# Kernel optimization log

Measured on AMD Instinct MI355X. Metric: run time of the kernel, lower is better.

Reference implementation:

```python
import jax, jax.numpy as jnp
import numpy as np

N_NODES = 100000


def setup_inputs() -> dict:
    key = jax.random.key(0)
    ks = jax.random.split(key, 8)
    nfeat, hdim, nclass, E = 512, 64, 256, 3200000
    x = jax.random.normal(ks[0], (N_NODES, nfeat), dtype=jnp.float32)
    edge_index = jax.random.randint(ks[1], (2, E), 0, N_NODES, dtype=jnp.int64)
    Win = jax.random.normal(ks[2], (nfeat, hdim), dtype=jnp.float32) * (1.0 / np.sqrt(nfeat))
    b_in = jnp.zeros((hdim,), dtype=jnp.float32)
    Wl = jax.random.normal(ks[3], (4, hdim, hdim), dtype=jnp.float32) * (1.0 / np.sqrt(hdim))
    bl = jnp.zeros((4, hdim), dtype=jnp.float32)
    Wr = jax.random.normal(ks[4], (4, hdim, hdim), dtype=jnp.float32) * (1.0 / np.sqrt(hdim))
    Wout = jax.random.normal(ks[5], (hdim, nclass), dtype=jnp.float32) * (1.0 / np.sqrt(hdim))
    b_out = jnp.zeros((nclass,), dtype=jnp.float32)
    return {"x": x, "edge_index": edge_index, "Win": Win, "b_in": b_in,
            "Wl": Wl, "bl": bl, "Wr": Wr, "Wout": Wout, "b_out": b_out}


def reference(x, edge_index, Win, b_in, Wl, bl, Wr, Wout, b_out):
    src, dst = edge_index[0], edge_index[1]
    # in-degree counts for scatter-mean (clamped to >=1 as in PyG)
    cnt = jax.ops.segment_sum(jnp.ones((src.shape[0],), dtype=x.dtype), dst,
                              num_segments=N_NODES)
    inv_cnt = (1.0 / jnp.maximum(cnt, 1.0))[:, None]  # [N,1]

    h = x @ Win + b_in  # [N, 64]
    for i in range(4):
        msg = h[src]  # gather neighbor features [E, 64]
        agg = jax.ops.segment_sum(msg, dst, num_segments=N_NODES) * inv_cnt
        conv = agg @ Wl[i] + bl[i] + h @ Wr[i]  # SAGEConv: lin_l(agg) + lin_r(h)
        h = h + jax.nn.relu(conv)  # residual
    return h @ Wout + b_out
```

## Files before the change

kernel.cpp:

```cpp
#include <hip/hip_runtime.h>
#include <hip/hip_bf16.h>

#define NN 100000
#define EE 3200000
#define HD 64
#define NF 512
#define NC 256

#define BSH 8
#define NB 391
#define EB 8192
#define NEB 391

typedef __attribute__((ext_vector_type(8))) short bf16x8;
typedef __attribute__((ext_vector_type(4))) float f32x4;
typedef __attribute__((ext_vector_type(4))) unsigned short u16x4;

__device__ __forceinline__ unsigned short f2bf(float f) {
    unsigned u = __float_as_uint(f);
    return (unsigned short)((u + 0x7FFFu + ((u >> 16) & 1u)) >> 16);
}
__device__ __forceinline__ unsigned pack2(float a, float b) {
    return (unsigned)f2bf(a) | ((unsigned)f2bf(b) << 16);
}
__device__ __forceinline__ float bf2f(unsigned short v) {
    return __uint_as_float(((unsigned)v) << 16);
}


__global__ __launch_bounds__(256) void part_count(const int* __restrict__ dst, int* __restrict__ hist) {
    __shared__ int hs[NB];
    int t = threadIdx.x, blk = blockIdx.x;
    for (int b = t; b < NB; b += 256) hs[b] = 0;
    __syncthreads();
    int base = blk * EB;
#pragma unroll
    for (int i = 0; i < EB / 256; ++i) {
        int e = base + t + 256 * i;
        if (e < EE) atomicAdd(&hs[dst[e] >> BSH], 1);
    }
    __syncthreads();
    for (int b = t; b < NB; b += 256) hist[blk * NB + b] = hs[b];
}


__global__ __launch_bounds__(512) void bucket_ptr(const int* __restrict__ hist, int* __restrict__ bucketptr) {
    __shared__ int s[512];
    int t = threadIdx.x;
    int v = 0;
    if (t < NB) {
        for (int blk = 0; blk < NEB; ++blk) v += hist[blk * NB + t];
    }
    s[t] = v; __syncthreads();
    for (int d = 1; d < 512; d <<= 1) {
        int a = (t >= d) ? s[t - d] : 0;
        __syncthreads();
        s[t] += a;
        __syncthreads();
    }
    if (t < NB) bucketptr[t] = s[t] - v;
    if (t == 0) bucketptr[NB] = EE;
}


__global__ __launch_bounds__(512) void part_scan(const int* __restrict__ hist, const int* __restrict__ bucketptr,
                                                 int* __restrict__ bboff) {
    __shared__ int s[512];
    int b = blockIdx.x, t = threadIdx.x;
    int v = (t < NEB) ? hist[t * NB + b] : 0;
    s[t] = v; __syncthreads();
    for (int d = 1; d < 512; d <<= 1) {
        int a = (t >= d) ? s[t - d] : 0;
        __syncthreads();
        s[t] += a;
        __syncthreads();
    }
    if (t < NEB) bboff[t * NB + b] = bucketptr[b] + s[t] - v;
}


__global__ __launch_bounds__(256) void part_scatter(const int* __restrict__ src, const int* __restrict__ dst,
                                                    const int* __restrict__ bboff, unsigned int* __restrict__ ebuf) {
    __shared__ int off[NB];
    __shared__ int rank[NB];
    int t = threadIdx.x, blk = blockIdx.x;
    for (int b = t; b < NB; b += 256) { off[b] = bboff[blk * NB + b]; rank[b] = 0; }
    __syncthreads();
    int base = blk * EB;
#pragma unroll
    for (int i = 0; i < EB / 256; ++i) {
        int e = base + t + 256 * i;
        if (e < EE) {
            int d = dst[e];
            int s = src[e];
            int b = d >> BSH;
            int r = atomicAdd(&rank[b], 1);
            ebuf[off[b] + r] = (unsigned)s | ((unsigned)(d & 255) << 17);
        }
    }
}


__global__ __launch_bounds__(256) void bucket_fill2(const unsigned int* __restrict__ ebuf,
                                                    const int* __restrict__ bucketptr,
                                                    int* __restrict__ rowptr, float* __restrict__ inv,
                                                    int* __restrict__ csr) {
    __shared__ int hcnt[256];
    __shared__ int scn[256];
    __shared__ int cur[256];
    int t = threadIdx.x, b = blockIdx.x;
    int n0 = b << BSH;
    hcnt[t] = 0;
    __syncthreads();
    int estart = bucketptr[b];
    int eend = bucketptr[b + 1];
    for (int e = estart + t; e < eend; e += 256) {
        atomicAdd(&hcnt[ebuf[e] >> 17], 1);
    }
    __syncthreads();
    int v = hcnt[t];
    scn[t] = v;
    __syncthreads();
    for (int d = 1; d < 256; d <<= 1) {
        int a = (t >= d) ? scn[t - d] : 0;
        __syncthreads();
        scn[t] += a;
        __syncthreads();
    }
    int off = estart + scn[t] - v;
    cur[t] = off;
    if (n0 + t < NN) {
        rowptr[n0 + t] = off;
        inv[n0 + t] = 1.0f / (float)(v > 1 ? v : 1);
    }
    if (b == NB - 1 && t == 0) rowptr[NN] = EE;
    __syncthreads();
    for (int e = estart + t; e < eend; e += 256) {
        unsigned u = ebuf[e];
        int dL = (int)(u >> 17);
        int p = atomicAdd(&cur[dL], 1);
        csr[p] = (int)(u & 0x1FFFFu);
    }
}


__global__ __launch_bounds__(256) void pack_w(const float* __restrict__ Win, unsigned short* __restrict__ wpk) {
    int id = blockIdx.x * 256 + threadIdx.x;
    int l = id & 63;
    int c = (id >> 6) & 3;
    int t = id >> 8;
    int kbase = t * 32 + (l >> 4) * 8;
    int col = c * 16 + (l & 15);
    float f[8];
#pragma unroll
    for (int j = 0; j < 8; ++j) f[j] = Win[(size_t)(kbase + j) * HD + col];
    uint4 p;
    p.x = pack2(f[0], f[1]); p.y = pack2(f[2], f[3]);
    p.z = pack2(f[4], f[5]); p.w = pack2(f[6], f[7]);
    *(uint4*)(wpk + (size_t)id * 8) = p;
}


__global__ __launch_bounds__(256) void gemm_in(const float* __restrict__ x, const unsigned short* __restrict__ wpk,
                                               const float* __restrict__ b_in, float* __restrict__ h,
                                               unsigned short* __restrict__ hb) {
    __shared__ unsigned short xs[128 * 64];
    int tid = threadIdx.x;
    int lane = tid & 63;
    int w = tid >> 6;
    int rowBase = blockIdx.x * 128;
    int lr = lane & 15;
    int lg = lane >> 4;

    f32x4 acc[2][4];
#pragma unroll
    for (int c = 0; c < 4; ++c) {
        float bb = b_in[c * 16 + lr];
#pragma unroll
        for (int m = 0; m < 2; ++m) acc[m][c] = (f32x4){bb, bb, bb, bb};
    }

    for (int kt = 0; kt < NF; kt += 64) {
        __syncthreads();
#pragma unroll
        for (int i = 0; i < 4; ++i) {
            int idx = tid + 256 * i;
            int r = idx >> 3;
            int u = idx & 7;
            int grow = rowBase + r;
            if (grow >= NN) grow = NN - 1;
            const float* srcp = x + (size_t)grow * NF + kt + u * 8;
            float4 a = *(const float4*)(srcp);
            float4 b = *(const float4*)(srcp + 4);
            uint4 p;
            p.x = pack2(a.x, a.y); p.y = pack2(a.z, a.w);
            p.z = pack2(b.x, b.y); p.w = pack2(b.z, b.w);
            int u2 = u ^ (r & 7);
            *(uint4*)(xs + (size_t)r * 64 + u2 * 8) = p;
        }
        __syncthreads();
#pragma unroll
        for (int ks = 0; ks < 2; ++ks) {
            int tstep = (kt >> 5) + ks;
            bf16x8 av[2], bv[4];
#pragma unroll
            for (int m = 0; m < 2; ++m) {
                int r = w * 32 + m * 16 + lr;
                int u2 = (ks * 4 + lg) ^ (r & 7);
                av[m] = *(const bf16x8*)(xs + (size_t)r * 64 + u2 * 8);
            }
#pragma unroll
            for (int c = 0; c < 4; ++c) {
                bv[c] = *(const bf16x8*)(wpk + (((size_t)tstep * 4 + c) * 64 + lane) * 8);
            }
#pragma unroll
            for (int m = 0; m < 2; ++m)
#pragma unroll
                for (int c = 0; c < 4; ++c)
                    acc[m][c] = __builtin_amdgcn_mfma_f32_16x16x32_bf16(av[m], bv[c], acc[m][c], 0, 0, 0);
        }
    }

#pragma unroll
    for (int m = 0; m < 2; ++m) {
        int rbase = rowBase + w * 32 + m * 16 + lg * 4;
#pragma unroll
        for (int j = 0; j < 4; ++j) {
            int row = rbase + j;
            if (row < NN) {
#pragma unroll
                for (int c = 0; c < 4; ++c) {
                    float v = acc[m][c][j];
                    h[(size_t)row * HD + c * 16 + lr] = v;
                    hb[(size_t)row * HD + c * 16 + lr] = f2bf(v);
                }
            }
        }
    }
}


__global__ __launch_bounds__(256) void aggregate(const unsigned short* __restrict__ hb, const int* __restrict__ rowptr,
                                                 const int* __restrict__ csr, const float* __restrict__ inv,
                                                 float4* __restrict__ agg4) {
    int tid = threadIdx.x;
    int lane = tid & 63;
    int q = lane >> 4;
    int f = lane & 15;
    int node = blockIdx.x * 4 + (tid >> 6);
    int n = __builtin_amdgcn_readfirstlane(node);
    int start = rowptr[n];
    int end = rowptr[n + 1];

    float4 acc0 = make_float4(0.f, 0.f, 0.f, 0.f);
    float4 acc1 = make_float4(0.f, 0.f, 0.f, 0.f);
    int e = start;
    int end8 = start + ((end - start) & ~7);
    for (; e < end8; e += 8) {
        int s0 = csr[e + q];
        int s1 = csr[e + 4 + q];
        u16x4 v0 = *(const u16x4*)(hb + (size_t)s0 * HD + f * 4);
        u16x4 v1 = *(const u16x4*)(hb + (size_t)s1 * HD + f * 4);
        acc0.x += bf2f(v0.x); acc0.y += bf2f(v0.y); acc0.z += bf2f(v0.z); acc0.w += bf2f(v0.w);
        acc1.x += bf2f(v1.x); acc1.y += bf2f(v1.y); acc1.z += bf2f(v1.z); acc1.w += bf2f(v1.w);
    }
    if (e + q < end) {
        int s = csr[e + q];
        u16x4 v = *(const u16x4*)(hb + (size_t)s * HD + f * 4);
        acc0.x += bf2f(v.x); acc0.y += bf2f(v.y); acc0.z += bf2f(v.z); acc0.w += bf2f(v.w);
    }
    e += 4;
    if (e + q < end) {
        int s = csr[e + q];
        u16x4 v = *(const u16x4*)(hb + (size_t)s * HD + f * 4);
        acc1.x += bf2f(v.x); acc1.y += bf2f(v.y); acc1.z += bf2f(v.z); acc1.w += bf2f(v.w);
    }

    float4 a;
    a.x = acc0.x + acc1.x;
    a.y = acc0.y + acc1.y;
    a.z = acc0.z + acc1.z;
    a.w = acc0.w + acc1.w;
    a.x += __shfl_xor(a.x, 16); a.x += __shfl_xor(a.x, 32);
    a.y += __shfl_xor(a.y, 16); a.y += __shfl_xor(a.y, 32);
    a.z += __shfl_xor(a.z, 16); a.z += __shfl_xor(a.z, 32);
    a.w += __shfl_xor(a.w, 16); a.w += __shfl_xor(a.w, 32);

    if (q == 0) {
        float s = inv[n];
        float4 r;
        r.x = a.x * s; r.y = a.y * s; r.z = a.z * s; r.w = a.w * s;
        agg4[(size_t)n * 16 + f] = r;
    }
}


__global__ __launch_bounds__(256) void layer_conv(const float* __restrict__ agg, float* __restrict__ h,
                                                  unsigned short* __restrict__ hb,
                                                  const float* __restrict__ Wl, const float* __restrict__ Wr,
                                                  const float* __restrict__ bl) {
    __shared__ float as_[64 * 64];
    __shared__ float hs[64 * 64];
    int tid = threadIdx.x;
    int cg = tid & 15;
    int rg = tid >> 4;
    int rowBase = blockIdx.x * 64;
    float4 bb = *(const float4*)(bl + cg * 4);
    float acc[4][4];
#pragma unroll
    for (int r = 0; r < 4; ++r) {
        acc[r][0] = bb.x; acc[r][1] = bb.y; acc[r][2] = bb.z; acc[r][3] = bb.w;
    }

#pragma unroll
    for (int i = 0; i < 4; ++i) {
        int idx = tid + 256 * i;
        int r = idx >> 4;
        int c4 = idx & 15;
        int grow = rowBase + r;
        if (grow >= NN) grow = NN - 1;
        int c4s = c4 ^ ((r >> 2) & 3);
        *(float4*)(as_ + r * 64 + c4s * 4) = *(const float4*)(agg + (size_t)grow * HD + c4 * 4);
        *(float4*)(hs + r * 64 + c4s * 4) = *(const float4*)(h + (size_t)grow * HD + c4 * 4);
    }
    __syncthreads();

#pragma unroll 2
    for (int k = 0; k < 64; k += 4) {
        int kq = k >> 2;
        float4 l0 = *(const float4*)(Wl + (size_t)(k + 0) * HD + cg * 4);
        float4 l1 = *(const float4*)(Wl + (size_t)(k + 1) * HD + cg * 4);
        float4 l2 = *(const float4*)(Wl + (size_t)(k + 2) * HD + cg * 4);
        float4 l3 = *(const float4*)(Wl + (size_t)(k + 3) * HD + cg * 4);
        float4 r0 = *(const float4*)(Wr + (size_t)(k + 0) * HD + cg * 4);
        float4 r1 = *(const float4*)(Wr + (size_t)(k + 1) * HD + cg * 4);
        float4 r2 = *(const float4*)(Wr + (size_t)(k + 2) * HD + cg * 4);
        float4 r3 = *(const float4*)(Wr + (size_t)(k + 3) * HD + cg * 4);
#pragma unroll
        for (int r = 0; r < 4; ++r) {
            int row = rg * 4 + r;
            int c4s = kq ^ ((row >> 2) & 3);
            float4 av = *(const float4*)(as_ + row * 64 + c4s * 4);
            float4 hv = *(const float4*)(hs + row * 64 + c4s * 4);
            acc[r][0] = fmaf(av.x, l0.x, acc[r][0]);
            acc[r][1] = fmaf(av.x, l0.y, acc[r][1]);
            acc[r][2] = fmaf(av.x, l0.z, acc[r][2]);
            acc[r][3] = fmaf(av.x, l0.w, acc[r][3]);
            acc[r][0] = fmaf(av.y, l1.x, acc[r][0]);
            acc[r][1] = fmaf(av.y, l1.y, acc[r][1]);
            acc[r][2] = fmaf(av.y, l1.z, acc[r][2]);
            acc[r][3] = fmaf(av.y, l1.w, acc[r][3]);
            acc[r][0] = fmaf(av.z, l2.x, acc[r][0]);
            acc[r][1] = fmaf(av.z, l2.y, acc[r][1]);
            acc[r][2] = fmaf(av.z, l2.z, acc[r][2]);
            acc[r][3] = fmaf(av.z, l2.w, acc[r][3]);
            acc[r][0] = fmaf(av.w, l3.x, acc[r][0]);
            acc[r][1] = fmaf(av.w, l3.y, acc[r][1]);
            acc[r][2] = fmaf(av.w, l3.z, acc[r][2]);
            acc[r][3] = fmaf(av.w, l3.w, acc[r][3]);
            acc[r][0] = fmaf(hv.x, r0.x, acc[r][0]);
            acc[r][1] = fmaf(hv.x, r0.y, acc[r][1]);
            acc[r][2] = fmaf(hv.x, r0.z, acc[r][2]);
            acc[r][3] = fmaf(hv.x, r0.w, acc[r][3]);
            acc[r][0] = fmaf(hv.y, r1.x, acc[r][0]);
            acc[r][1] = fmaf(hv.y, r1.y, acc[r][1]);
            acc[r][2] = fmaf(hv.y, r1.z, acc[r][2]);
            acc[r][3] = fmaf(hv.y, r1.w, acc[r][3]);
            acc[r][0] = fmaf(hv.z, r2.x, acc[r][0]);
            acc[r][1] = fmaf(hv.z, r2.y, acc[r][1]);
            acc[r][2] = fmaf(hv.z, r2.z, acc[r][2]);
            acc[r][3] = fmaf(hv.z, r2.w, acc[r][3]);
            acc[r][0] = fmaf(hv.w, r3.x, acc[r][0]);
            acc[r][1] = fmaf(hv.w, r3.y, acc[r][1]);
            acc[r][2] = fmaf(hv.w, r3.z, acc[r][2]);
            acc[r][3] = fmaf(hv.w, r3.w, acc[r][3]);
        }
    }

#pragma unroll
    for (int r = 0; r < 4; ++r) {
        int row = rowBase + rg * 4 + r;
        if (row < NN) {
            int lrow = rg * 4 + r;
            int c4s = cg ^ ((lrow >> 2) & 3);
            float4 ho = *(const float4*)(hs + lrow * 64 + c4s * 4);
            float4 o;
            float c0 = acc[r][0], c1 = acc[r][1], c2 = acc[r][2], c3 = acc[r][3];
            o.x = ho.x + (c0 > 0.f ? c0 : 0.f);
            o.y = ho.y + (c1 > 0.f ? c1 : 0.f);
            o.z = ho.z + (c2 > 0.f ? c2 : 0.f);
            o.w = ho.w + (c3 > 0.f ? c3 : 0.f);
            *(float4*)(h + (size_t)row * HD + cg * 4) = o;
            u16x4 ob;
            ob.x = f2bf(o.x); ob.y = f2bf(o.y); ob.z = f2bf(o.z); ob.w = f2bf(o.w);
            *(u16x4*)(hb + (size_t)row * HD + cg * 4) = ob;
        }
    }
}


__global__ __launch_bounds__(256) void gemm_out_k(const float* __restrict__ h, const float* __restrict__ Wout,
                                                  const float* __restrict__ b_out, float* __restrict__ out) {
    __shared__ float hs[32 * 64];
    int tid = threadIdx.x;
    int cg = tid & 63;
    int rg = tid >> 6;
    int rowBase = blockIdx.x * 32;
#pragma unroll
    for (int i = 0; i < 2; ++i) {
        int idx = tid + 256 * i;
        int r = idx >> 4;
        int c4 = idx & 15;
        int grow = rowBase + r;
        if (grow >= NN) grow = NN - 1;
        *(float4*)(hs + r * 64 + c4 * 4) = *(const float4*)(h + (size_t)grow * HD + c4 * 4);
    }
    __syncthreads();

    float4 bb = *(const float4*)(b_out + cg * 4);
    float acc[8][4];
#pragma unroll
    for (int r = 0; r < 8; ++r) {
        acc[r][0] = bb.x; acc[r][1] = bb.y; acc[r][2] = bb.z; acc[r][3] = bb.w;
    }

#pragma unroll 2
    for (int k = 0; k < 64; k += 4) {
        float4 w0 = *(const float4*)(Wout + (size_t)(k + 0) * NC + cg * 4);
        float4 w1 = *(const float4*)(Wout + (size_t)(k + 1) * NC + cg * 4);
        float4 w2 = *(const float4*)(Wout + (size_t)(k + 2) * NC + cg * 4);
        float4 w3 = *(const float4*)(Wout + (size_t)(k + 3) * NC + cg * 4);
#pragma unroll
        for (int r = 0; r < 8; ++r) {
            float4 hv = *(const float4*)(hs + (rg * 8 + r) * 64 + k);
            acc[r][0] = fmaf(hv.x, w0.x, acc[r][0]);
            acc[r][1] = fmaf(hv.x, w0.y, acc[r][1]);
            acc[r][2] = fmaf(hv.x, w0.z, acc[r][2]);
            acc[r][3] = fmaf(hv.x, w0.w, acc[r][3]);
            acc[r][0] = fmaf(hv.y, w1.x, acc[r][0]);
            acc[r][1] = fmaf(hv.y, w1.y, acc[r][1]);
            acc[r][2] = fmaf(hv.y, w1.z, acc[r][2]);
            acc[r][3] = fmaf(hv.y, w1.w, acc[r][3]);
            acc[r][0] = fmaf(hv.z, w2.x, acc[r][0]);
            acc[r][1] = fmaf(hv.z, w2.y, acc[r][1]);
            acc[r][2] = fmaf(hv.z, w2.z, acc[r][2]);
            acc[r][3] = fmaf(hv.z, w2.w, acc[r][3]);
            acc[r][0] = fmaf(hv.w, w3.x, acc[r][0]);
            acc[r][1] = fmaf(hv.w, w3.y, acc[r][1]);
            acc[r][2] = fmaf(hv.w, w3.z, acc[r][2]);
            acc[r][3] = fmaf(hv.w, w3.w, acc[r][3]);
        }
    }
#pragma unroll
    for (int r = 0; r < 8; ++r) {
        int row = rowBase + rg * 8 + r;
        if (row < NN) {
            float4 o;
            o.x = acc[r][0]; o.y = acc[r][1]; o.z = acc[r][2]; o.w = acc[r][3];
            *(float4*)(out + (size_t)row * NC + cg * 4) = o;
        }
    }
}

extern "C" void kernel_launch(void* const* d_in, const int* in_sizes, int n_in,
                              void* d_out, int out_size, void* d_ws, size_t ws_size,
                              hipStream_t stream) {
    const float* x    = (const float*)d_in[0];
    const int*   ei   = (const int*)d_in[1];
    const float* Win  = (const float*)d_in[2];
    const float* b_in = (const float*)d_in[3];
    const float* Wl   = (const float*)d_in[4];
    const float* bl   = (const float*)d_in[5];
    const float* Wr   = (const float*)d_in[6];
    const float* Wout = (const float*)d_in[7];
    const float* b_out= (const float*)d_in[8];
    float* out = (float*)d_out;

    const int* src = ei;
    const int* dst = ei + EE;

    char* ws = (char*)d_ws;
    float* h        = (float*)ws;
    float* agg      = h + (size_t)NN * HD;
    int*   rowptr   = (int*)(agg + (size_t)NN * HD);
    int*   csr      = rowptr + 100004;
    float* inv      = (float*)(csr + EE);
    int*   bucketptr= (int*)(inv + NN);
    unsigned short* wpk = (unsigned short*)(bucketptr + 400);
    unsigned short* hbf = wpk + 32768;

    unsigned int* ebuf = (unsigned int*)agg;
    int* hist  = (int*)agg + EE;
    int* bboff = hist + NEB * NB;

    pack_w<<<16, 256, 0, stream>>>(Win, wpk);

    part_count<<<NEB, 256, 0, stream>>>(dst, hist);
    bucket_ptr<<<1, 512, 0, stream>>>(hist, bucketptr);
    part_scan<<<NB, 512, 0, stream>>>(hist, bucketptr, bboff);
    part_scatter<<<NEB, 256, 0, stream>>>(src, dst, bboff, ebuf);
    bucket_fill2<<<NB, 256, 0, stream>>>(ebuf, bucketptr, rowptr, inv, csr);

    gemm_in<<<(NN + 127) / 128, 256, 0, stream>>>(x, wpk, b_in, h, hbf);

    for (int i = 0; i < 4; ++i) {
        aggregate<<<NN / 4, 256, 0, stream>>>(hbf, rowptr, csr, inv, (float4*)agg);
        layer_conv<<<(NN + 63) / 64, 256, 0, stream>>>(agg, h, hbf, Wl + (size_t)i * HD * HD,
                                                       Wr + (size_t)i * HD * HD, bl + (size_t)i * HD);
    }

    gemm_out_k<<<(NN + 31) / 32, 256, 0, stream>>>(h, Wout, b_out, out);
}
```

Before: 1.004 ms.

## Fuse aggregation with SAGE conv via bf16 MFMA and use MFMA output GEMM

New measurement: 901.3 us. 10.2% less time.

```diff
diff --git a/kernel.cpp b/kernel.cpp
--- a/kernel.cpp
+++ b/kernel.cpp
@@ -42,7 +42,6 @@
     __syncthreads();
     for (int b = t; b < NB; b += 256) hist[blk * NB + b] = hs[b];
 }
-
 
 __global__ __launch_bounds__(512) void bucket_ptr(const int* __restrict__ hist, int* __restrict__ bucketptr) {
     __shared__ int s[512];
@@ -61,7 +60,6 @@
     if (t < NB) bucketptr[t] = s[t] - v;
     if (t == 0) bucketptr[NB] = EE;
 }
-
 
 __global__ __launch_bounds__(512) void part_scan(const int* __restrict__ hist, const int* __restrict__ bucketptr,
                                                  int* __restrict__ bboff) {
@@ -78,7 +76,6 @@
     if (t < NEB) bboff[t * NB + b] = bucketptr[b] + s[t] - v;
 }
 
-
 __global__ __launch_bounds__(256) void part_scatter(const int* __restrict__ src, const int* __restrict__ dst,
                                                     const int* __restrict__ bboff, unsigned int* __restrict__ ebuf) {
     __shared__ int off[NB];
@@ -99,7 +96,6 @@
         }
     }
 }
-
 
 __global__ __launch_bounds__(256) void bucket_fill2(const unsigned int* __restrict__ ebuf,
                                                     const int* __restrict__ bucketptr,
@@ -158,6 +154,44 @@
     p.x = pack2(f[0], f[1]); p.y = pack2(f[2], f[3]);
     p.z = pack2(f[4], f[5]); p.w = pack2(f[6], f[7]);
     *(uint4*)(wpk + (size_t)id * 8) = p;
+}
+
+__global__ __launch_bounds__(256) void pack_wl(const float* __restrict__ Wl, const float* __restrict__ Wr,
+                                               unsigned short* __restrict__ wlpk) {
+    int id = blockIdx.x * 256 + threadIdx.x;
+    int l = id & 63;
+    int c = (id >> 6) & 3;
+    int t = (id >> 8) & 3;
+    int i = id >> 10;
+    int kbase = t * 32 + (l >> 4) * 8;
+    int col = c * 16 + (l & 15);
+    float f[8];
+#pragma unroll
+    for (int j = 0; j < 8; ++j) {
+        int k = kbase + j;
+        f[j] = (k < 64) ? Wl[(size_t)i * 4096 + (size_t)k * HD + col]
+                        : Wr[(size_t)i * 4096 + (size_t)(k - 64) * HD + col];
+    }
+    uint4 p;
+    p.x = pack2(f[0], f[1]); p.y = pack2(f[2], f[3]);
+    p.z = pack2(f[4], f[5]); p.w = pack2(f[6], f[7]);
+    *(uint4*)(wlpk + (size_t)id * 8) = p;
+}
+
+__global__ __launch_bounds__(256) void pack_wout(const float* __restrict__ Wout, unsigned short* __restrict__ wopk) {
+    int id = blockIdx.x * 256 + threadIdx.x;
+    int l = id & 63;
+    int c = (id >> 6) & 15;
+    int t = id >> 10;
+    int kbase = t * 32 + (l >> 4) * 8;
+    int col = c * 16 + (l & 15);
+    float f[8];
+#pragma unroll
+    for (int j = 0; j < 8; ++j) f[j] = Wout[(size_t)(kbase + j) * NC + col];
+    uint4 p;
+    p.x = pack2(f[0], f[1]); p.y = pack2(f[2], f[3]);
+    p.z = pack2(f[4], f[5]); p.w = pack2(f[6], f[7]);
+    *(uint4*)(wopk + (size_t)id * 8) = p;
 }
 
 
@@ -240,17 +274,25 @@
 }
 
 
-__global__ __launch_bounds__(256) void aggregate(const unsigned short* __restrict__ hb, const int* __restrict__ rowptr,
-                                                 const int* __restrict__ csr, const float* __restrict__ inv,
-                                                 float4* __restrict__ agg4) {
+__global__ __launch_bounds__(1024) void layer_fused(const float* __restrict__ hin,
+                                                    const unsigned short* __restrict__ hbin,
+                                                    const int* __restrict__ rowptr, const int* __restrict__ csr,
+                                                    const float* __restrict__ inv,
+                                                    const unsigned short* __restrict__ wlpk,
+                                                    const float* __restrict__ bl,
+                                                    float* __restrict__ hout, unsigned short* __restrict__ hbout) {
+    __shared__ unsigned short a_bf[16 * 64];
+    __shared__ unsigned short h_bf[16 * 64];
+    __shared__ float h_f[16 * 64];
     int tid = threadIdx.x;
+    int w = tid >> 6;
     int lane = tid & 63;
+    int node = __builtin_amdgcn_readfirstlane(blockIdx.x * 16 + w);
+
     int q = lane >> 4;
     int f = lane & 15;
-    int node = blockIdx.x * 4 + (tid >> 6);
-    int n = __builtin_amdgcn_readfirstlane(node);
-    int start = rowptr[n];
-    int end = rowptr[n + 1];
+    int start = rowptr[node];
+    int end = rowptr[node + 1];
 
     float4 acc0 = make_float4(0.f, 0.f, 0.f, 0.f);
     float4 acc1 = make_float4(0.f, 0.f, 0.f, 0.f);
@@ -259,23 +301,22 @@
     for (; e < end8; e += 8) {
         int s0 = csr[e + q];
         int s1 = csr[e + 4 + q];
-        u16x4 v0 = *(const u16x4*)(hb + (size_t)s0 * HD + f * 4);
-        u16x4 v1 = *(const u16x4*)(hb + (size_t)s1 * HD + f * 4);
+        u16x4 v0 = *(const u16x4*)(hbin + (size_t)s0 * HD + f * 4);
+        u16x4 v1 = *(const u16x4*)(hbin + (size_t)s1 * HD + f * 4);
         acc0.x += bf2f(v0.x); acc0.y += bf2f(v0.y); acc0.z += bf2f(v0.z); acc0.w += bf2f(v0.w);
         acc1.x += bf2f(v1.x); acc1.y += bf2f(v1.y); acc1.z += bf2f(v1.z); acc1.w += bf2f(v1.w);
     }
     if (e + q < end) {
         int s = csr[e + q];
-        u16x4 v = *(const u16x4*)(hb + (size_t)s * HD + f * 4);
+        u16x4 v = *(const u16x4*)(hbin + (size_t)s * HD + f * 4);
         acc0.x += bf2f(v.x); acc0.y += bf2f(v.y); acc0.z += bf2f(v.z); acc0.w += bf2f(v.w);
     }
     e += 4;
     if (e + q < end) {
         int s = csr[e + q];
-        u16x4 v = *(const u16x4*)(hb + (size_t)s * HD + f * 4);
+        u16x4 v = *(const u16x4*)(hbin + (size_t)s * HD + f * 4);
         acc1.x += bf2f(v.x); acc1.y += bf2f(v.y); acc1.z += bf2f(v.z); acc1.w += bf2f(v.w);
     }
-
     float4 a;
     a.x = acc0.x + acc1.x;
     a.y = acc0.y + acc1.y;
@@ -285,179 +326,83 @@
     a.y += __shfl_xor(a.y, 16); a.y += __shfl_xor(a.y, 32);
     a.z += __shfl_xor(a.z, 16); a.z += __shfl_xor(a.z, 32);
     a.w += __shfl_xor(a.w, 16); a.w += __shfl_xor(a.w, 32);
-
     if (q == 0) {
-        float s = inv[n];
-        float4 r;
-        r.x = a.x * s; r.y = a.y * s; r.z = a.z * s; r.w = a.w * s;
-        agg4[(size_t)n * 16 + f] = r;
-    }
-}
-
-
-__global__ __launch_bounds__(256) void layer_conv(const float* __restrict__ agg, float* __restrict__ h,
-                                                  unsigned short* __restrict__ hb,
-                                                  const float* __restrict__ Wl, const float* __restrict__ Wr,
-                                                  const float* __restrict__ bl) {
-    __shared__ float as_[64 * 64];
-    __shared__ float hs[64 * 64];
+        float s = inv[node];
+        int u = f >> 1;
+        int u2 = u ^ (w & 7);
+        u16x4 ob;
+        ob.x = f2bf(a.x * s); ob.y = f2bf(a.y * s); ob.z = f2bf(a.z * s); ob.w = f2bf(a.w * s);
+        *(u16x4*)(a_bf + w * 64 + u2 * 8 + (f & 1) * 4) = ob;
+    }
+    {
+        float hv = hin[(size_t)node * HD + lane];
+        h_f[w * 64 + lane] = hv;
+        int u = lane >> 3;
+        int u2 = u ^ (w & 7);
+        h_bf[w * 64 + u2 * 8 + (lane & 7)] = f2bf(hv);
+    }
+    __syncthreads();
+
+    if (w < 4) {
+        int c = w;
+        int lr = lane & 15;
+        int lg = lane >> 4;
+        float bb = bl[c * 16 + lr];
+        f32x4 acc = (f32x4){bb, bb, bb, bb};
+#pragma unroll
+        for (int t = 0; t < 4; ++t) {
+            const unsigned short* asrc = (t < 2) ? a_bf : h_bf;
+            int ks = t & 1;
+            int u2 = (ks * 4 + lg) ^ (lr & 7);
+            bf16x8 av = *(const bf16x8*)(asrc + (size_t)lr * 64 + u2 * 8);
+            bf16x8 bv = *(const bf16x8*)(wlpk + (((size_t)t * 4 + c) * 64 + lane) * 8);
+            acc = __builtin_amdgcn_mfma_f32_16x16x32_bf16(av, bv, acc, 0, 0, 0);
+        }
+#pragma unroll
+        for (int j = 0; j < 4; ++j) {
+            int nl = lg * 4 + j;
+            int gnode = blockIdx.x * 16 + nl;
+            float ho = h_f[nl * 64 + c * 16 + lr];
+            float cv = acc[j];
+            float o = ho + (cv > 0.f ? cv : 0.f);
+            hout[(size_t)gnode * HD + c * 16 + lr] = o;
+            hbout[(size_t)gnode * HD + c * 16 + lr] = f2bf(o);
+        }
+    }
+}
+
+
+__global__ __launch_bounds__(256) void gemm_out_m(const unsigned short* __restrict__ hb,
+                                                  const unsigned short* __restrict__ wopk,
+                                                  const float* __restrict__ b_out, float* __restrict__ out) {
     int tid = threadIdx.x;
-    int cg = tid & 15;
-    int rg = tid >> 4;
-    int rowBase = blockIdx.x * 64;
-    float4 bb = *(const float4*)(bl + cg * 4);
-    float acc[4][4];
-#pragma unroll
-    for (int r = 0; r < 4; ++r) {
-        acc[r][0] = bb.x; acc[r][1] = bb.y; acc[r][2] = bb.z; acc[r][3] = bb.w;
-    }
-
-#pragma unroll
-    for (int i = 0; i < 4; ++i) {
-        int idx = tid + 256 * i;
-        int r = idx >> 4;
-        int c4 = idx & 15;
-        int grow = rowBase + r;
-        if (grow >= NN) grow = NN - 1;
-        int c4s = c4 ^ ((r >> 2) & 3);
-        *(float4*)(as_ + r * 64 + c4s * 4) = *(const float4*)(agg + (size_t)grow * HD + c4 * 4);
-        *(float4*)(hs + r * 64 + c4s * 4) = *(const float4*)(h + (size_t)grow * HD + c4 * 4);
-    }
-    __syncthreads();
-
-#pragma unroll 2
-    for (int k = 0; k < 64; k += 4) {
-        int kq = k >> 2;
-        float4 l0 = *(const float4*)(Wl + (size_t)(k + 0) * HD + cg * 4);
-        float4 l1 = *(const float4*)(Wl + (size_t)(k + 1) * HD + cg * 4);
-        float4 l2 = *(const float4*)(Wl + (size_t)(k + 2) * HD + cg * 4);
-        float4 l3 = *(const float4*)(Wl + (size_t)(k + 3) * HD + cg * 4);
-        float4 r0 = *(const float4*)(Wr + (size_t)(k + 0) * HD + cg * 4);
-        float4 r1 = *(const float4*)(Wr + (size_t)(k + 1) * HD + cg * 4);
-        float4 r2 = *(const float4*)(Wr + (size_t)(k + 2) * HD + cg * 4);
-        float4 r3 = *(const float4*)(Wr + (size_t)(k + 3) * HD + cg * 4);
-#pragma unroll
-        for (int r = 0; r < 4; ++r) {
-            int row = rg * 4 + r;
-            int c4s = kq ^ ((row >> 2) & 3);
-            float4 av = *(const float4*)(as_ + row * 64 + c4s * 4);
-            float4 hv = *(const float4*)(hs + row * 64 + c4s * 4);
-            acc[r][0] = fmaf(av.x, l0.x, acc[r][0]);
-            acc[r][1] = fmaf(av.x, l0.y, acc[r][1]);
-            acc[r][2] = fmaf(av.x, l0.z, acc[r][2]);
-            acc[r][3] = fmaf(av.x, l0.w, acc[r][3]);
-            acc[r][0] = fmaf(av.y, l1.x, acc[r][0]);
-            acc[r][1] = fmaf(av.y, l1.y, acc[r][1]);
-            acc[r][2] = fmaf(av.y, l1.z, acc[r][2]);
-            acc[r][3] = fmaf(av.y, l1.w, acc[r][3]);
-            acc[r][0] = fmaf(av.z, l2.x, acc[r][0]);
-            acc[r][1] = fmaf(av.z, l2.y, acc[r][1]);
-            acc[r][2] = fmaf(av.z, l2.z, acc[r][2]);
-            acc[r][3] = fmaf(av.z, l2.w, acc[r][3]);
-            acc[r][0] = fmaf(av.w, l3.x, acc[r][0]);
-            acc[r][1] = fmaf(av.w, l3.y, acc[r][1]);
-            acc[r][2] = fmaf(av.w, l3.z, acc[r][2]);
-            acc[r][3] = fmaf(av.w, l3.w, acc[r][3]);
-            acc[r][0] = fmaf(hv.x, r0.x, acc[r][0]);
-            acc[r][1] = fmaf(hv.x, r0.y, acc[r][1]);
-            acc[r][2] = fmaf(hv.x, r0.z, acc[r][2]);
-            acc[r][3] = fmaf(hv.x, r0.w, acc[r][3]);
-            acc[r][0] = fmaf(hv.y, r1.x, acc[r][0]);
-            acc[r][1] = fmaf(hv.y, r1.y, acc[r][1]);
-            acc[r][2] = fmaf(hv.y, r1.z, acc[r][2]);
-            acc[r][3] = fmaf(hv.y, r1.w, acc[r][3]);
-            acc[r][0] = fmaf(hv.z, r2.x, acc[r][0]);
-            acc[r][1] = fmaf(hv.z, r2.y, acc[r][1]);
-            acc[r][2] = fmaf(hv.z, r2.z, acc[r][2]);
-            acc[r][3] = fmaf(hv.z, r2.w, acc[r][3]);
-            acc[r][0] = fmaf(hv.w, r3.x, acc[r][0]);
-            acc[r][1] = fmaf(hv.w, r3.y, acc[r][1]);
-            acc[r][2] = fmaf(hv.w, r3.z, acc[r][2]);
-            acc[r][3] = fmaf(hv.w, r3.w, acc[r][3]);
-        }
-    }
-
-#pragma unroll
-    for (int r = 0; r < 4; ++r) {
-        int row = rowBase + rg * 4 + r;
-        if (row < NN) {
-            int lrow = rg * 4 + r;
-            int c4s = cg ^ ((lrow >> 2) & 3);
-            float4 ho = *(const float4*)(hs + lrow * 64 + c4s * 4);
-            float4 o;
-            float c0 = acc[r][0], c1 = acc[r][1], c2 = acc[r][2], c3 = acc[r][3];
-            o.x = ho.x + (c0 > 0.f ? c0 : 0.f);
-            o.y = ho.y + (c1 > 0.f ? c1 : 0.f);
-            o.z = ho.z + (c2 > 0.f ? c2 : 0.f);
-            o.w = ho.w + (c3 > 0.f ? c3 : 0.f);
-            *(float4*)(h + (size_t)row * HD + cg * 4) = o;
-            u16x4 ob;
-            ob.x = f2bf(o.x); ob.y = f2bf(o.y); ob.z = f2bf(o.z); ob.w = f2bf(o.w);
-            *(u16x4*)(hb + (size_t)row * HD + cg * 4) = ob;
-        }
-    }
-}
-
-
-__global__ __launch_bounds__(256) void gemm_out_k(const float* __restrict__ h, const float* __restrict__ Wout,
-                                                  const float* __restrict__ b_out, float* __restrict__ out) {
-    __shared__ float hs[32 * 64];
-    int tid = threadIdx.x;
-    int cg = tid & 63;
-    int rg = tid >> 6;
-    int rowBase = blockIdx.x * 32;
-#pragma unroll
-    for (int i = 0; i < 2; ++i) {
-        int idx = tid + 256 * i;
-        int r = idx >> 4;
-        int c4 = idx & 15;
-        int grow = rowBase + r;
-        if (grow >= NN) grow = NN - 1;
-        *(float4*)(hs + r * 64 + c4 * 4) = *(const float4*)(h + (size_t)grow * HD + c4 * 4);
-    }
-    __syncthreads();
-
-    float4 bb = *(const float4*)(b_out + cg * 4);
-    float acc[8][4];
-#pragma unroll
-    for (int r = 0; r < 8; ++r) {
-        acc[r][0] = bb.x; acc[r][1] = bb.y; acc[r][2] = bb.z; acc[r][3] = bb.w;
-    }
-
-#pragma unroll 2
-    for (int k = 0; k < 64; k += 4) {
-        float4 w0 = *(const float4*)(Wout + (size_t)(k + 0) * NC + cg * 4);
-        float4 w1 = *(const float4*)(Wout + (size_t)(k + 1) * NC + cg * 4);
-        float4 w2 = *(const float4*)(Wout + (size_t)(k + 2) * NC + cg * 4);
-        float4 w3 = *(const float4*)(Wout + (size_t)(k + 3) * NC + cg * 4);
-#pragma unroll
-        for (int r = 0; r < 8; ++r) {
-            float4 hv = *(const float4*)(hs + (rg * 8 + r) * 64 + k);
-            acc[r][0] = fmaf(hv.x, w0.x, acc[r][0]);
-            acc[r][1] = fmaf(hv.x, w0.y, acc[r][1]);
-            acc[r][2] = fmaf(hv.x, w0.z, acc[r][2]);
-            acc[r][3] = fmaf(hv.x, w0.w, acc[r][3]);
-            acc[r][0] = fmaf(hv.y, w1.x, acc[r][0]);
-            acc[r][1] = fmaf(hv.y, w1.y, acc[r][1]);
-            acc[r][2] = fmaf(hv.y, w1.z, acc[r][2]);
-            acc[r][3] = fmaf(hv.y, w1.w, acc[r][3]);
-            acc[r][0] = fmaf(hv.z, w2.x, acc[r][0]);
-            acc[r][1] = fmaf(hv.z, w2.y, acc[r][1]);
-            acc[r][2] = fmaf(hv.z, w2.z, acc[r][2]);
-            acc[r][3] = fmaf(hv.z, w2.w, acc[r][3]);
-            acc[r][0] = fmaf(hv.w, w3.x, acc[r][0]);
-            acc[r][1] = fmaf(hv.w, w3.y, acc[r][1]);
-            acc[r][2] = fmaf(hv.w, w3.z, acc[r][2]);
-            acc[r][3] = fmaf(hv.w, w3.w, acc[r][3]);
-        }
-    }
-#pragma unroll
-    for (int r = 0; r < 8; ++r) {
-        int row = rowBase + rg * 8 + r;
-        if (row < NN) {
-            float4 o;
-            o.x = acc[r][0]; o.y = acc[r][1]; o.z = acc[r][2]; o.w = acc[r][3];
-            *(float4*)(out + (size_t)row * NC + cg * 4) = o;
+    int lane = tid & 63;
+    int w = tid >> 6;
+    int rowBase = blockIdx.x * 64 + w * 16;
+    int lr = lane & 15;
+    int lg = lane >> 4;
+
+    int row = rowBase + lr;
+    int rrow = (row < NN) ? row : NN - 1;
+    bf16x8 av0 = *(const bf16x8*)(hb + (size_t)rrow * HD + lg * 8);
+    bf16x8 av1 = *(const bf16x8*)(hb + (size_t)rrow * HD + 32 + lg * 8);
+
+    f32x4 acc[16];
+#pragma unroll
+    for (int c = 0; c < 16; ++c) {
+        float bb = b_out[c * 16 + lr];
+        acc[c] = (f32x4){bb, bb, bb, bb};
+        bf16x8 b0 = *(const bf16x8*)(wopk + (((size_t)0 * 16 + c) * 64 + lane) * 8);
+        bf16x8 b1 = *(const bf16x8*)(wopk + (((size_t)1 * 16 + c) * 64 + lane) * 8);
+        acc[c] = __builtin_amdgcn_mfma_f32_16x16x32_bf16(av0, b0, acc[c], 0, 0, 0);
+        acc[c] = __builtin_amdgcn_mfma_f32_16x16x32_bf16(av1, b1, acc[c], 0, 0, 0);
+    }
+#pragma unroll
+    for (int c = 0; c < 16; ++c) {
+#pragma unroll
+        for (int j = 0; j < 4; ++j) {
+            int r = rowBase + lg * 4 + j;
+            if (r < NN) out[(size_t)r * NC + c * 16 + lr] = acc[c][j];
         }
     }
 }
@@ -480,20 +425,25 @@
     const int* dst = ei + EE;
 
     char* ws = (char*)d_ws;
-    float* h        = (float*)ws;
-    float* agg      = h + (size_t)NN * HD;
-    int*   rowptr   = (int*)(agg + (size_t)NN * HD);
+    float* h0       = (float*)ws;
+    float* h1       = h0 + (size_t)NN * HD;
+    int*   rowptr   = (int*)(h1 + (size_t)NN * HD);
     int*   csr      = rowptr + 100004;
     float* inv      = (float*)(csr + EE);
     int*   bucketptr= (int*)(inv + NN);
-    unsigned short* wpk = (unsigned short*)(bucketptr + 400);
-    unsigned short* hbf = wpk + 32768;
-
-    unsigned int* ebuf = (unsigned int*)agg;
-    int* hist  = (int*)agg + EE;
+    unsigned short* wpk  = (unsigned short*)(bucketptr + 400);
+    unsigned short* wlpk = wpk + 32768;
+    unsigned short* wopk = wlpk + 32768;
+    unsigned short* hb0  = wopk + 16384;
+    unsigned short* hb1  = hb0 + (size_t)NN * HD;
+
+    unsigned int* ebuf = (unsigned int*)h1;
+    int* hist  = (int*)h1 + EE;
     int* bboff = hist + NEB * NB;
 
     pack_w<<<16, 256, 0, stream>>>(Win, wpk);
+    pack_wl<<<16, 256, 0, stream>>>(Wl, Wr, wlpk);
+    pack_wout<<<8, 256, 0, stream>>>(Wout, wopk);
 
     part_count<<<NEB, 256, 0, stream>>>(dst, hist);
     bucket_ptr<<<1, 512, 0, stream>>>(hist, bucketptr);
@@ -501,13 +451,16 @@
     part_scatter<<<NEB, 256, 0, stream>>>(src, dst, bboff, ebuf);
     bucket_fill2<<<NB, 256, 0, stream>>>(ebuf, bucketptr, rowptr, inv, csr);
 
-    gemm_in<<<(NN + 127) / 128, 256, 0, stream>>>(x, wpk, b_in, h, hbf);
-
+    gemm_in<<<(NN + 127) / 128, 256, 0, stream>>>(x, wpk, b_in, h0, hb0);
+
+    float* hA = h0; unsigned short* hbA = hb0;
+    float* hB = h1; unsigned short* hbB = hb1;
     for (int i = 0; i < 4; ++i) {
-        aggregate<<<NN / 4, 256, 0, stream>>>(hbf, rowptr, csr, inv, (float4*)agg);
-        layer_conv<<<(NN + 63) / 64, 256, 0, stream>>>(agg, h, hbf, Wl + (size_t)i * HD * HD,
-                                                       Wr + (size_t)i * HD * HD, bl + (size_t)i * HD);
-    }
-
-    gemm_out_k<<<(NN + 31) / 32, 256, 0, stream>>>(h, Wout, b_out, out);
-}
+        layer_fused<<<NN / 16, 1024, 0, stream>>>(hA, hbA, rowptr, csr, inv,
+                                                  wlpk + (size_t)i * 8192, bl + (size_t)i * HD, hB, hbB);
+        float* tf = hA; hA = hB; hB = tf;
+        unsigned short* tb = hbA; hbA = hbB; hbB = tb;
+    }
+
+    gemm_out_m<<<(NN + 63) / 64, 256, 0, stream>>>(hbA, wopk, b_out, out);
+}
```
